# Performance work log

Measured on AMD Instinct MI355X. Metric: run time of the kernel, lower is better.

The kernel has to match this reference:

```python
import jax, jax.numpy as jnp
import numpy as np
from jax import lax

SHIFT = 32  # shift_range from init
EPS_NORM = 1e-12
EPS_MASK = 1e-6


def _l2_normalize_flat(x):
    # F.normalize(x.reshape(B,-1)): per-sample L2 normalize with eps 1e-12
    B = x.shape[0]
    flat = x.reshape(B, -1)
    n = jnp.linalg.norm(flat, axis=1, keepdims=True)
    return (flat / jnp.maximum(n, EPS_NORM)).reshape(x.shape)


def setup_inputs() -> dict:
    key = jax.random.key(0)
    k1, k2 = jax.random.split(key)
    grd_feature = jax.random.normal(k1, (8, 32, 32, 32), dtype=jnp.float32)
    sat_feature = jax.random.normal(k2, (8, 32, 128, 128), dtype=jnp.float32)
    return {"grd_feature": grd_feature, "sat_feature": sat_feature, "test_method": 1}


def reference(grd_feature, sat_feature, test_method):
    # test_method == 1 path (default); test_method in {0,1} only differ in divisor
    M, C, H_s, W_s = sat_feature.shape
    N, _, H, W = grd_feature.shape
    kH = min(H, H_s - 2 * SHIFT)
    kW = min(W, W_s - 2 * SHIFT)

    # center-crop ground template to (kH, kW) and L2-normalize per sample
    gh0, gw0 = H // 2 - kH // 2, W // 2 - kW // 2
    grd = grd_feature[:, :, gh0:gh0 + 2 * (kH // 2), gw0:gw0 + 2 * (kW // 2)]
    N_, _, H_k, W_k = grd.shape
    grd = _l2_normalize_flat(grd)

    # center-crop satellite to search region and L2-normalize per sample
    sh0 = H_s // 2 - SHIFT - kH // 2
    sw0 = W_s // 2 - SHIFT - kW // 2
    sat = sat_feature[:, :, sh0:sh0 + 2 * (SHIFT + kH // 2), sw0:sw0 + 2 * (SHIFT + kW // 2)]
    _, _, H_i, W_i = sat.shape
    sat = _l2_normalize_flat(sat)

    # all-pairs cross-correlation: corr[m, n, y, x] (torch grouped-conv on repeated sat
    # is equivalent to a plain VALID conv of sat with all N ground filters)
    corr = lax.conv_general_dilated(
        sat, grd, window_strides=(1, 1), padding='VALID',
        dimension_numbers=('NCHW', 'OIHW', 'NCHW'))  # [M, N, Ho, Wo]
    Ho, Wo = corr.shape[2], corr.shape[3]

    # sliding-window sum of |sat|^2 (avg_pool with divisor_override=1, summed over C)
    s2 = jnp.sum(sat * sat, axis=1)  # [M, H_i, W_i]
    partical = lax.reduce_window(s2, jnp.float32(0), lax.add,
                                 (1, H_k, W_k), (1, 1, 1), 'VALID')  # [M, Ho, Wo]
    if test_method == 0:
        denom = jnp.sqrt(partical)
    else:
        denom = partical
    corr = corr / jnp.maximum(denom[:, None], EPS_NORM)

    similarity_matrix = jnp.max(corr, axis=(2, 3))  # [M, N]

    # diagonal pairs (m == n): peak localization
    diag = jnp.diagonal(corr, axis1=0, axis2=1)        # [Ho, Wo, M]
    diag = jnp.transpose(diag, (2, 0, 1)).reshape(M, -1)
    max_index = jnp.argmax(diag, axis=-1)
    pos_h = max_index // Wo
    pos_w = max_index % Wo

    grd_mask = (jnp.abs(jnp.sum(grd, axis=1)) > EPS_MASK).astype(jnp.float32)  # [N, H_k, W_k]

    def place(ph, pw, gm):
        z = jnp.zeros((1, H_i, W_i), dtype=jnp.float32)
        return lax.dynamic_update_slice(z, gm[None], (0, ph, pw))

    mask = jax.vmap(place)(pos_h, pos_w, grd_mask)  # [M, 1, H_i, W_i]
    return similarity_matrix, mask
```

## Files before the change

### kernel.cpp

```cpp
#include <hip/hip_runtime.h>
#include <stdint.h>

typedef unsigned short u16;
typedef unsigned int u32;
typedef __bf16 bf16x8 __attribute__((ext_vector_type(8)));
typedef float floatx4 __attribute__((ext_vector_type(4)));

#define DEVI static __device__ __forceinline__

DEVI u16 f2bf(float f) {
  uint32_t u = __builtin_bit_cast(uint32_t, f);
  u += 0x7FFFu + ((u >> 16) & 1u);
  return (u16)(u >> 16);
}
DEVI float bf2f(u16 b) { return __builtin_bit_cast(float, (uint32_t)b << 16); }

static constexpr size_t OFF_CORRP = 0;
static constexpr size_t OFF_SATT  = OFF_CORRP + (size_t)4*270400*4;
static constexpr size_t OFF_GRDP  = OFF_SATT + (size_t)8*4*96*96*8*2;
static constexpr size_t OFF_S2    = OFF_GRDP + (size_t)4*1024*16*8*2;
static constexpr size_t OFF_NRMP  = OFF_S2   + (size_t)73728*4;
static constexpr size_t OFF_GNRM  = OFF_NRMP + 8*48*4;
static constexpr size_t OFF_MASK  = OFF_GNRM + 32;

__global__ void k_prep(const float* __restrict__ grd, const float* __restrict__ sat,
                       u16* __restrict__ sTh, u16* __restrict__ gP,
                       float* __restrict__ s2, float* __restrict__ nrmp,
                       float* __restrict__ gnrm, float* __restrict__ gmask) {
  __shared__ float L[2*32*97];
  __shared__ float red[256];
  const int t = threadIdx.x;
  if (blockIdx.x < 384) {
    const int m  = blockIdx.x / 48;
    const int yp = blockIdx.x - (blockIdx.x / 48) * 48;
    #pragma unroll
    for (int k = 0; k < 6; ++k) {
      const int idx = k*256 + t;
      const int row = idx / 768;
      const int r2  = idx - row*768;
      const int c   = r2 / 24;
      const int xq  = r2 - c*24;
      const int y   = yp*2 + row;
      const float4 v = *(const float4*)(sat + (((size_t)m*32 + c)*128 + (16+y))*128 + 16 + xq*4);
      float* Lp = &L[(row*32 + c)*97 + xq*4];
      Lp[0]=v.x; Lp[1]=v.y; Lp[2]=v.z; Lp[3]=v.w;
    }
    __syncthreads();
    float ss = 0.f;
    if (t < 192) {
      const int row = t / 96, x = t - (t/96)*96;
      #pragma unroll
      for (int c = 0; c < 32; ++c) { const float v = L[(row*32+c)*97 + x]; ss += v*v; }
      s2[(size_t)m*9216 + (yp*2+row)*96 + x] = ss;
    }
    red[t] = ss; __syncthreads();
    for (int s = 128; s > 0; s >>= 1) { if (t < s) red[t] += red[t+s]; __syncthreads(); }
    if (t == 0) nrmp[m*48 + yp] = red[0];
    #pragma unroll
    for (int k = 0; k < 3; ++k) {
      const int o   = k*256 + t;
      const int row = o / 384;
      const int r2  = o - row*384;
      const int cb  = r2 / 96;
      const int x   = r2 - cb*96;
      union { u16 us[8]; uint4 v4; } P;
      #pragma unroll
      for (int e = 0; e < 8; ++e) P.us[e] = f2bf(L[(row*32 + cb*8 + e)*97 + x]);
      *(uint4*)(&sTh[(((size_t)m*4+cb)*9216 + (size_t)(yp*2+row)*96 + x)*8]) = P.v4;
    }
  } else {
    const int n = blockIdx.x - 384;
    float nn = 0.f, scs[4];
    #pragma unroll
    for (int it = 0; it < 4; ++it) {
      const int pidx = it*256 + t;
      float vals[32]; float sc = 0.f;
      #pragma unroll
      for (int c = 0; c < 32; ++c) {
        const float v = grd[((size_t)n*32 + c)*1024 + pidx];
        vals[c] = v; sc += v; nn += v*v;
      }
      scs[it] = sc;
      #pragma unroll
      for (int cb = 0; cb < 4; ++cb) {
        union { u16 us[8]; uint4 v4; } ph, pl;
        #pragma unroll
        for (int e = 0; e < 8; ++e) {
          const float v = vals[cb*8+e];
          const u16 h = f2bf(v); ph.us[e] = h; pl.us[e] = f2bf(v - bf2f(h));
        }
        const size_t o = ((size_t)cb*1024 + pidx)*128;
        *(uint4*)(&gP[o + (size_t)n*8])     = ph.v4;
        *(uint4*)(&gP[o + (size_t)(n+8)*8]) = pl.v4;
      }
    }
    red[t] = nn; __syncthreads();
    for (int s = 128; s > 0; s >>= 1) { if (t < s) red[t] += red[t+s]; __syncthreads(); }
    const float gn = fmaxf(sqrtf(red[0]), 1e-12f);
    if (t == 0) gnrm[n] = red[0];
    const float thr = 1e-6f * gn;
    #pragma unroll
    for (int it = 0; it < 4; ++it)
      gmask[n*1024 + it*256 + t] = (fabsf(scs[it]) > thr) ? 1.f : 0.f;
  }
}

__global__ __launch_bounds__(256, 4) void k_conv(
    const u16* __restrict__ satT, const u16* __restrict__ gP,
    float* __restrict__ corr_p)
{
  __shared__ __align__(16) u16 patch[36*48*8];

  int bi = blockIdx.x;
  const int cb = bi & 3; bi >>= 2;
  const int xt = bi % 5; bi /= 5;
  const int yt = bi % 13;
  const int m  = bi / 13;
  const int y0 = yt*5, x0 = xt*16;
  const int tid = threadIdx.x;
  const int wave = tid >> 6, lane = tid & 63;

  {
    const size_t rowbase = ((size_t)(m*4 + cb) * 96 + y0) * 96;
    for (int k = tid; k < 36*48; k += 256) {
      const int rho = k / 48;
      const int px  = k - rho*48;
      int X = x0 + px; if (X > 95) X = 95;
      *(uint4*)(&patch[(size_t)k*8]) = *(const uint4*)(&satT[(rowbase + (size_t)rho*96 + X)*8]);
    }
  }
  __syncthreads();

  const int pr = lane & 15;
  const int q  = lane >> 4;

  floatx4 acc[5];
  #pragma unroll
  for (int r = 0; r < 5; ++r) acc[r] = (floatx4){0.f, 0.f, 0.f, 0.f};

  #pragma unroll
  for (int jbi = 0; jbi < 2; ++jbi) {
    const int jb = wave*2 + jbi;
    const int apx = pr + jb*4 + q;
    const u16* bp = gP + ((size_t)cb*1024 + (size_t)(jb*4+q))*128 + (size_t)pr*8;

    uint4 Br[8];
    #pragma unroll
    for (int ii = 0; ii < 8; ++ii) Br[ii] = *(const uint4*)(bp + (size_t)ii*4096);
    uint4 Ah[8];
    #pragma unroll
    for (int s = 0; s < 6; ++s) Ah[s] = *(const uint4*)(&patch[((size_t)s*48 + apx)*8]);

    #pragma unroll
    for (int i = 0; i < 32; ++i) {
      if (i < 30)
        Ah[(i+6)&7] = *(const uint4*)(&patch[((size_t)(i+6)*48 + apx)*8]);
      const bf16x8 bf = __builtin_bit_cast(bf16x8, Br[i&7]);
      if (i < 24)
        Br[(i+8)&7] = *(const uint4*)(bp + (size_t)(i+8)*4096);
      #pragma unroll
      for (int r = 0; r < 5; ++r)
        acc[r] = __builtin_amdgcn_mfma_f32_16x16x32_bf16(
            __builtin_bit_cast(bf16x8, Ah[(i+r)&7]), bf, acc[r], 0, 0, 0);
    }
  }

  float vals[20];
  #pragma unroll
  for (int r = 0; r < 5; ++r)
    #pragma unroll
    for (int e = 0; e < 4; ++e)
      vals[r*4+e] = acc[r][e] + __shfl_xor(acc[r][e], 8);

  __syncthreads();
  float* red = (float*)patch;
  #pragma unroll
  for (int u = 0; u < 20; ++u) red[((size_t)wave*64 + lane)*21 + u] = vals[u];
  __syncthreads();
  if (wave == 0 && pr < 8) {
    #pragma unroll
    for (int r = 0; r < 5; ++r) {
      #pragma unroll
      for (int e = 0; e < 4; ++e) {
        const int x = x0 + q*4 + e;
        if (x < 65) {
          float s = 0.f;
          #pragma unroll
          for (int w = 0; w < 4; ++w) s += red[((size_t)w*64 + lane)*21 + r*4 + e];
          corr_p[(size_t)cb*270400 + ((size_t)(m*8+pr)*65 + (y0+r))*65 + x] = s;
        }
      }
    }
  }
}

__global__ __launch_bounds__(256) void k_post(
    const float* __restrict__ corr_p, const float* __restrict__ s2,
    const float* __restrict__ nrmp, const float* __restrict__ gnrm,
    const int* __restrict__ tm, const float* __restrict__ grd,
    const float* __restrict__ sat, const float* __restrict__ gmask,
    float* __restrict__ out)
{
  __shared__ float bufA[9216];
  __shared__ float bufB[6240];
  __shared__ float red[256];
  __shared__ int cands[64];
  __shared__ int ccnt;
  __shared__ float sbest; __shared__ int sbix;

  const int m = blockIdx.x >> 3, n = blockIdx.x & 7, t = threadIdx.x;

  red[t] = (t < 48) ? nrmp[m*48 + t] : 0.f;
  __syncthreads();
  for (int s = 128; s > 0; s >>= 1) { if (t < s) red[t] += red[t+s]; __syncthreads(); }
  const float srn = 1.f / fmaxf(sqrtf(red[0]), 1e-12f);
  const float grn = 1.f / fmaxf(sqrtf(gnrm[n]), 1e-12f);
  const float cscale = grn * srn, pscale = srn * srn;
  const int method = tm[0];

  for (int idx = t; idx < 9216; idx += 256) bufA[idx] = s2[(size_t)m*9216 + idx];
  __syncthreads();
  for (int idx = t; idx < 6240; idx += 256) {
    const int y = idx / 65, xo = idx - y*65;
    const float* r = &bufA[y*96 + xo];
    float s = 0.f;
    #pragma unroll
    for (int j = 0; j < 32; ++j) s += r[j];
    bufB[idx] = s;
  }
  __syncthreads();
  for (int idx = t; idx < 4225; idx += 256) {
    const int yo = idx / 65, xo = idx - yo*65;
    float s = 0.f;
    #pragma unroll
    for (int i = 0; i < 32; ++i) s += bufB[(yo+i)*65 + xo];
    bufA[idx] = s;
  }
  __syncthreads();
  const float* cp = corr_p + (size_t)(m*8+n)*4225;
  float bestv = -3.4e38f;
  for (int idx = t; idx < 4225; idx += 256) {
    const float c = cp[idx] + cp[idx+270400] + cp[idx+540800] + cp[idx+811200];
    const float pt = bufA[idx] * pscale;
    float denom = (method == 0) ? sqrtf(pt) : pt;
    denom = fmaxf(denom, 1e-12f);
    const float v = c * cscale / denom;
    bufB[idx] = v;
    bestv = fmaxf(bestv, v);
  }
  __syncthreads();
  red[t] = bestv; __syncthreads();
  for (int s = 128; s > 0; s >>= 1) { if (t < s) red[t] = fmaxf(red[t], red[t+s]); __syncthreads(); }
  if (t == 0) out[m*8 + n] = red[0];
  if (m != n) return;
  const float vmax = red[0];

  if (t == 0) { ccnt = 0; sbest = -3.4e38f; sbix = 0x7FFFFFFF; }
  __syncthreads();
  const float thr = vmax - 3e-3f;
  for (int idx = t; idx < 4225; idx += 256)
    if (bufB[idx] >= thr) { const int s = atomicAdd(&ccnt, 1); if (s < 64) cands[s] = idx; }
  __syncthreads();
  int nc = ccnt; if (nc > 64) nc = 64; if (nc < 1) nc = 1;

  const int c = t >> 3, s8 = t & 7;
  for (int ci = 0; ci < nc; ++ci) {
    const int idx = cands[ci];
    const int y = idx / 65, x = idx - y*65;
    float a = 0.f;
    #pragma unroll
    for (int ii = 0; ii < 4; ++ii) {
      const int i = s8 + ii*8;
      const float* gr = grd + ((size_t)n*32 + c)*1024 + i*32;
      const float* sr = sat + (((size_t)n*32 + c)*128 + (16 + y + i))*128 + (16 + x);
      #pragma unroll
      for (int j = 0; j < 32; ++j) a += gr[j] * sr[j];
    }
    red[t] = a; __syncthreads();
    for (int st = 128; st > 0; st >>= 1) { if (t < st) red[t] += red[t+st]; __syncthreads(); }
    if (t == 0) {
      const float pt = bufA[idx] * pscale;
      float denom = (method == 0) ? sqrtf(pt) : pt;
      denom = fmaxf(denom, 1e-12f);
      const float v = red[0] * cscale / denom;
      if (v > sbest || (v == sbest && idx < sbix)) { sbest = v; sbix = idx; }
    }
    __syncthreads();
  }
  const int bix = sbix;
  const int ph = bix / 65, pw = bix - (bix/65)*65;
  for (int p = t; p < 1024; p += 256)
    out[64 + (size_t)n*9216 + (size_t)(ph + (p>>5))*96 + (pw + (p&31))] = gmask[n*1024 + p];
}

extern "C" void kernel_launch(void* const* d_in, const int* in_sizes, int n_in,
                              void* d_out, int out_size, void* d_ws, size_t ws_size,
                              hipStream_t stream) {
  const float* grd = (const float*)d_in[0];
  const float* sat = (const float*)d_in[1];
  const int*   tm  = (const int*)d_in[2];
  float* out = (float*)d_out;
  char* ws = (char*)d_ws;

  float* corrp = (float*)(ws + OFF_CORRP);
  u16*   sTh   = (u16*)(ws + OFF_SATT);
  u16*   gP    = (u16*)(ws + OFF_GRDP);
  float* s2    = (float*)(ws + OFF_S2);
  float* nrmp  = (float*)(ws + OFF_NRMP);
  float* gnrm  = (float*)(ws + OFF_GNRM);
  float* gmask = (float*)(ws + OFF_MASK);

  hipMemsetAsync(d_out, 0, (size_t)out_size * sizeof(float), stream);

  k_prep<<<392,  256, 0, stream>>>(grd, sat, sTh, gP, s2, nrmp, gnrm, gmask);
  k_conv<<<2080, 256, 0, stream>>>(sTh, gP, corrp);
  k_post<<<64,   256, 0, stream>>>(corrp, s2, nrmp, gnrm, tm, grd, sat, gmask, out);
}
```

Measured before the change: 170.8 us.

## Split post-processing into parallel vmax and output kernels, move window sums into conv

The single 64-block post kernel, which recomputed the sliding-window |sat|^2 sums per (m,n) pair, is replaced. The window sums are now computed once per sample by 72 extra blocks appended to the conv launch. The normalize-and-max step is spread over 320 blocks writing partial maxima, and a small 9-block kernel finishes the reduction and candidate refinement. The prep kernel also processes one row per block instead of two, doubling its grid. The aim is to remove the redundant window-sum work and the poor parallelism of the old tail kernel, at the cost of an extra launch and a workspace round trip for the diagonal values.

```diff
diff --git a/kernel.cpp b/kernel.cpp
--- a/kernel.cpp
+++ b/kernel.cpp
@@ -19,57 +19,49 @@
 static constexpr size_t OFF_SATT  = OFF_CORRP + (size_t)4*270400*4;
 static constexpr size_t OFF_GRDP  = OFF_SATT + (size_t)8*4*96*96*8*2;
 static constexpr size_t OFF_S2    = OFF_GRDP + (size_t)4*1024*16*8*2;
-static constexpr size_t OFF_NRMP  = OFF_S2   + (size_t)73728*4;
-static constexpr size_t OFF_GNRM  = OFF_NRMP + 8*48*4;
+static constexpr size_t OFF_PART  = OFF_S2   + (size_t)73728*4;
+static constexpr size_t OFF_NRMP  = OFF_PART + (size_t)33800*4;
+static constexpr size_t OFF_GNRM  = OFF_NRMP + 768*4;
 static constexpr size_t OFF_MASK  = OFF_GNRM + 32;
-
-__global__ void k_prep(const float* __restrict__ grd, const float* __restrict__ sat,
-                       u16* __restrict__ sTh, u16* __restrict__ gP,
-                       float* __restrict__ s2, float* __restrict__ nrmp,
-                       float* __restrict__ gnrm, float* __restrict__ gmask) {
-  __shared__ float L[2*32*97];
+static constexpr size_t OFF_VDIAG = OFF_MASK + (size_t)8192*4;
+static constexpr size_t OFF_PMAX  = OFF_VDIAG + (size_t)33800*4;
+
+__global__ __launch_bounds__(256) void k_prep(
+    const float* __restrict__ grd, const float* __restrict__ sat,
+    u16* __restrict__ sTh, u16* __restrict__ gP,
+    float* __restrict__ s2, float* __restrict__ nrmp,
+    float* __restrict__ gnrm, float* __restrict__ gmask) {
+  __shared__ float L[32*100];
   __shared__ float red[256];
   const int t = threadIdx.x;
-  if (blockIdx.x < 384) {
-    const int m  = blockIdx.x / 48;
-    const int yp = blockIdx.x - (blockIdx.x / 48) * 48;
-    #pragma unroll
-    for (int k = 0; k < 6; ++k) {
+  if (blockIdx.x < 768) {
+    const int m = blockIdx.x / 96, y = blockIdx.x - (blockIdx.x / 96) * 96;
+    #pragma unroll
+    for (int k = 0; k < 3; ++k) {
       const int idx = k*256 + t;
-      const int row = idx / 768;
-      const int r2  = idx - row*768;
-      const int c   = r2 / 24;
-      const int xq  = r2 - c*24;
-      const int y   = yp*2 + row;
+      const int c = idx / 24, xq = idx - c*24;
       const float4 v = *(const float4*)(sat + (((size_t)m*32 + c)*128 + (16+y))*128 + 16 + xq*4);
-      float* Lp = &L[(row*32 + c)*97 + xq*4];
-      Lp[0]=v.x; Lp[1]=v.y; Lp[2]=v.z; Lp[3]=v.w;
+      *(float4*)(&L[c*100 + xq*4]) = v;
     }
     __syncthreads();
     float ss = 0.f;
-    if (t < 192) {
-      const int row = t / 96, x = t - (t/96)*96;
-      #pragma unroll
-      for (int c = 0; c < 32; ++c) { const float v = L[(row*32+c)*97 + x]; ss += v*v; }
-      s2[(size_t)m*9216 + (yp*2+row)*96 + x] = ss;
+    if (t < 96) {
+      #pragma unroll
+      for (int c = 0; c < 32; ++c) { const float v = L[c*100 + t]; ss += v*v; }
+      s2[(size_t)m*9216 + y*96 + t] = ss;
     }
     red[t] = ss; __syncthreads();
     for (int s = 128; s > 0; s >>= 1) { if (t < s) red[t] += red[t+s]; __syncthreads(); }
-    if (t == 0) nrmp[m*48 + yp] = red[0];
-    #pragma unroll
-    for (int k = 0; k < 3; ++k) {
-      const int o   = k*256 + t;
-      const int row = o / 384;
-      const int r2  = o - row*384;
-      const int cb  = r2 / 96;
-      const int x   = r2 - cb*96;
+    if (t == 0) nrmp[m*96 + y] = red[0];
+    for (int idx = t; idx < 384; idx += 256) {
+      const int cb = idx / 96, x = idx - cb*96;
       union { u16 us[8]; uint4 v4; } P;
       #pragma unroll
-      for (int e = 0; e < 8; ++e) P.us[e] = f2bf(L[(row*32 + cb*8 + e)*97 + x]);
-      *(uint4*)(&sTh[(((size_t)m*4+cb)*9216 + (size_t)(yp*2+row)*96 + x)*8]) = P.v4;
+      for (int e = 0; e < 8; ++e) P.us[e] = f2bf(L[(cb*8+e)*100 + x]);
+      *(uint4*)(&sTh[(((size_t)m*4+cb)*9216 + (size_t)y*96 + x)*8]) = P.v4;
     }
   } else {
-    const int n = blockIdx.x - 384;
+    const int n = blockIdx.x - 768;
     float nn = 0.f, scs[4];
     #pragma unroll
     for (int it = 0; it < 4; ++it) {
@@ -107,17 +99,49 @@
 
 __global__ __launch_bounds__(256, 4) void k_conv(
     const u16* __restrict__ satT, const u16* __restrict__ gP,
-    float* __restrict__ corr_p)
+    const float* __restrict__ s2, float* __restrict__ corr_p,
+    float* __restrict__ part)
 {
   __shared__ __align__(16) u16 patch[36*48*8];
 
   int bi = blockIdx.x;
+  const int tid = threadIdx.x;
+
+  if (bi >= 2080) {
+    float* S  = (float*)patch;
+    float* HS = S + 40*96;
+    const int pb = bi - 2080;
+    const int pm = pb / 9, ysl = (pb - pm*9)*8;
+    const int nrows = (65 - ysl) < 8 ? (65 - ysl) : 8;
+    const int scnt  = (96 - ysl) < 40 ? (96 - ysl) : 40;
+    for (int idx = tid; idx < scnt*96; idx += 256)
+      S[idx] = s2[(size_t)pm*9216 + (size_t)ysl*96 + idx];
+    __syncthreads();
+    const int hrows = nrows + 31;
+    for (int idx = tid; idx < hrows*65; idx += 256) {
+      const int r = idx / 65, xo = idx - r*65;
+      const float* p = &S[r*96 + xo];
+      float s = 0.f;
+      #pragma unroll
+      for (int j = 0; j < 32; ++j) s += p[j];
+      HS[idx] = s;
+    }
+    __syncthreads();
+    for (int idx = tid; idx < nrows*65; idx += 256) {
+      const int r = idx / 65, xo = idx - r*65;
+      float s = 0.f;
+      #pragma unroll
+      for (int i = 0; i < 32; ++i) s += HS[(r+i)*65 + xo];
+      part[(size_t)pm*4225 + (size_t)(ysl+r)*65 + xo] = s;
+    }
+    return;
+  }
+
   const int cb = bi & 3; bi >>= 2;
   const int xt = bi % 5; bi /= 5;
   const int yt = bi % 13;
   const int m  = bi / 13;
   const int y0 = yt*5, x0 = xt*16;
-  const int tid = threadIdx.x;
   const int wave = tid >> 6, lane = tid & 63;
 
   {
@@ -194,72 +218,83 @@
   }
 }
 
-__global__ __launch_bounds__(256) void k_post(
-    const float* __restrict__ corr_p, const float* __restrict__ s2,
+__global__ __launch_bounds__(256) void k_vmax(
+    const float* __restrict__ corr_p, const float* __restrict__ part,
     const float* __restrict__ nrmp, const float* __restrict__ gnrm,
-    const int* __restrict__ tm, const float* __restrict__ grd,
-    const float* __restrict__ sat, const float* __restrict__ gmask,
-    float* __restrict__ out)
+    const int* __restrict__ tm, float* __restrict__ vdiag,
+    float* __restrict__ pmax)
 {
-  __shared__ float bufA[9216];
-  __shared__ float bufB[6240];
   __shared__ float red[256];
-  __shared__ int cands[64];
-  __shared__ int ccnt;
-  __shared__ float sbest; __shared__ int sbix;
-
-  const int m = blockIdx.x >> 3, n = blockIdx.x & 7, t = threadIdx.x;
-
-  red[t] = (t < 48) ? nrmp[m*48 + t] : 0.f;
+  const int bi = blockIdx.x;
+  const int m = bi / 40, n = (bi / 5) & 7, yc = bi % 5;
+  const int t = threadIdx.x;
+  red[t] = (t < 96) ? nrmp[m*96 + t] : 0.f;
   __syncthreads();
   for (int s = 128; s > 0; s >>= 1) { if (t < s) red[t] += red[t+s]; __syncthreads(); }
   const float srn = 1.f / fmaxf(sqrtf(red[0]), 1e-12f);
   const float grn = 1.f / fmaxf(sqrtf(gnrm[n]), 1e-12f);
   const float cscale = grn * srn, pscale = srn * srn;
   const int method = tm[0];
-
-  for (int idx = t; idx < 9216; idx += 256) bufA[idx] = s2[(size_t)m*9216 + idx];
-  __syncthreads();
-  for (int idx = t; idx < 6240; idx += 256) {
-    const int y = idx / 65, xo = idx - y*65;
-    const float* r = &bufA[y*96 + xo];
-    float s = 0.f;
-    #pragma unroll
-    for (int j = 0; j < 32; ++j) s += r[j];
-    bufB[idx] = s;
-  }
-  __syncthreads();
-  for (int idx = t; idx < 4225; idx += 256) {
-    const int yo = idx / 65, xo = idx - yo*65;
-    float s = 0.f;
-    #pragma unroll
-    for (int i = 0; i < 32; ++i) s += bufB[(yo+i)*65 + xo];
-    bufA[idx] = s;
-  }
-  __syncthreads();
   const float* cp = corr_p + (size_t)(m*8+n)*4225;
+  const float* pp = part + (size_t)m*4225;
+  const int i0 = yc*845, i1 = i0 + 845;
+  const bool diag = (m == n);
   float bestv = -3.4e38f;
-  for (int idx = t; idx < 4225; idx += 256) {
+  for (int idx = i0 + t; idx < i1; idx += 256) {
     const float c = cp[idx] + cp[idx+270400] + cp[idx+540800] + cp[idx+811200];
-    const float pt = bufA[idx] * pscale;
+    const float pt = pp[idx] * pscale;
     float denom = (method == 0) ? sqrtf(pt) : pt;
     denom = fmaxf(denom, 1e-12f);
     const float v = c * cscale / denom;
-    bufB[idx] = v;
+    if (diag) vdiag[(size_t)m*4225 + idx] = v;
     bestv = fmaxf(bestv, v);
   }
   __syncthreads();
   red[t] = bestv; __syncthreads();
   for (int s = 128; s > 0; s >>= 1) { if (t < s) red[t] = fmaxf(red[t], red[t+s]); __syncthreads(); }
-  if (t == 0) out[m*8 + n] = red[0];
-  if (m != n) return;
-  const float vmax = red[0];
-
+  if (t == 0) pmax[bi] = red[0];
+}
+
+__global__ __launch_bounds__(256) void k_out(
+    const float* __restrict__ vdiag, const float* __restrict__ pmax,
+    const float* __restrict__ grd, const float* __restrict__ sat,
+    const float* __restrict__ part, const float* __restrict__ nrmp,
+    const float* __restrict__ gnrm, const int* __restrict__ tm,
+    const float* __restrict__ gmask, float* __restrict__ out)
+{
+  const int t = threadIdx.x;
+  if (blockIdx.x == 8) {
+    if (t < 64) {
+      float v = pmax[t*5];
+      #pragma unroll
+      for (int k = 1; k < 5; ++k) v = fmaxf(v, pmax[t*5 + k]);
+      out[t] = v;
+    }
+    return;
+  }
+  const int n = blockIdx.x;
+  __shared__ float red[256];
+  __shared__ int cands[64];
+  __shared__ int ccnt;
+  __shared__ float sbest; __shared__ int sbix;
+
+  red[t] = (t < 96) ? nrmp[n*96 + t] : 0.f;
+  __syncthreads();
+  for (int s = 128; s > 0; s >>= 1) { if (t < s) red[t] += red[t+s]; __syncthreads(); }
+  const float srn = 1.f / fmaxf(sqrtf(red[0]), 1e-12f);
+  const float grn = 1.f / fmaxf(sqrtf(gnrm[n]), 1e-12f);
+  const float cscale = grn * srn, pscale = srn * srn;
+  const int method = tm[0];
+
+  float vm = pmax[n*45];
+  #pragma unroll
+  for (int k = 1; k < 5; ++k) vm = fmaxf(vm, pmax[n*45 + k]);
   if (t == 0) { ccnt = 0; sbest = -3.4e38f; sbix = 0x7FFFFFFF; }
   __syncthreads();
-  const float thr = vmax - 3e-3f;
+  const float thr = vm - 3e-3f;
+  const float* vd = vdiag + (size_t)n*4225;
   for (int idx = t; idx < 4225; idx += 256)
-    if (bufB[idx] >= thr) { const int s = atomicAdd(&ccnt, 1); if (s < 64) cands[s] = idx; }
+    if (vd[idx] >= thr) { const int s = atomicAdd(&ccnt, 1); if (s < 64) cands[s] = idx; }
   __syncthreads();
   int nc = ccnt; if (nc > 64) nc = 64; if (nc < 1) nc = 1;
 
@@ -279,7 +314,7 @@
     red[t] = a; __syncthreads();
     for (int st = 128; st > 0; st >>= 1) { if (t < st) red[t] += red[t+st]; __syncthreads(); }
     if (t == 0) {
-      const float pt = bufA[idx] * pscale;
+      const float pt = part[(size_t)n*4225 + idx] * pscale;
       float denom = (method == 0) ? sqrtf(pt) : pt;
       denom = fmaxf(denom, 1e-12f);
       const float v = red[0] * cscale / denom;
@@ -306,13 +341,17 @@
   u16*   sTh   = (u16*)(ws + OFF_SATT);
   u16*   gP    = (u16*)(ws + OFF_GRDP);
   float* s2    = (float*)(ws + OFF_S2);
+  float* part  = (float*)(ws + OFF_PART);
   float* nrmp  = (float*)(ws + OFF_NRMP);
   float* gnrm  = (float*)(ws + OFF_GNRM);
   float* gmask = (float*)(ws + OFF_MASK);
+  float* vdiag = (float*)(ws + OFF_VDIAG);
+  float* pmax  = (float*)(ws + OFF_PMAX);
 
   hipMemsetAsync(d_out, 0, (size_t)out_size * sizeof(float), stream);
 
-  k_prep<<<392,  256, 0, stream>>>(grd, sat, sTh, gP, s2, nrmp, gnrm, gmask);
-  k_conv<<<2080, 256, 0, stream>>>(sTh, gP, corrp);
-  k_post<<<64,   256, 0, stream>>>(corrp, s2, nrmp, gnrm, tm, grd, sat, gmask, out);
-}
+  k_prep<<<776,  256, 0, stream>>>(grd, sat, sTh, gP, s2, nrmp, gnrm, gmask);
+  k_conv<<<2152, 256, 0, stream>>>(sTh, gP, s2, corrp, part);
+  k_vmax<<<320,  256, 0, stream>>>(corrp, part, nrmp, gnrm, tm, vdiag, pmax);
+  k_out <<<9,    256, 0, stream>>>(vdiag, pmax, grd, sat, part, nrmp, gnrm, tm, gmask, out);
+}
```

Measured after the change: 154.5 us. 9.6% less time.
